# Optimization experiments

Measured on AMD Instinct MI355X. Metric: run time of the kernel, lower is better.

The kernel has to match this reference:

```python
import jax, jax.numpy as jnp
import numpy as np
import math

H = 16          # head_count
D = 1024        # model_dim
DT = 100        # topic_dim
DH = D // H     # dim_per_head


def _lin(x, W, b):
    return x @ W.T + b


def _shape(x, B):
    # [B, L, D] -> [B, H, L, DH]
    return x.reshape(B, -1, H, DH).transpose(0, 2, 1, 3)


def setup_inputs() -> dict:
    key = jax.random.key(0)
    ks = jax.random.split(key, 20)
    B, L = 4, 1024
    s = 0.02
    inp = {
        'key': jax.random.normal(ks[0], (B, L, D), jnp.float32),
        'value': jax.random.normal(ks[1], (B, L, D), jnp.float32),
        'query': jax.random.normal(ks[2], (B, L, D), jnp.float32),
        'mask': jax.random.randint(ks[3], (B, L, L), 0, 2).astype(bool),
        'topic_vec': jax.random.normal(ks[4], (B, L, DT), jnp.float32),
        'Wq': jax.random.normal(ks[5], (D, D), jnp.float32) * s,
        'bq': jnp.zeros((D,), jnp.float32),
        'Wk': jax.random.normal(ks[6], (D, D), jnp.float32) * s,
        'bk': jnp.zeros((D,), jnp.float32),
        'Wv': jax.random.normal(ks[7], (D, D), jnp.float32) * s,
        'bv': jnp.zeros((D,), jnp.float32),
        'Wtk': jax.random.normal(ks[8], (D, D), jnp.float32) * s,
        'btk': jnp.zeros((D,), jnp.float32),
        'Wtv': jax.random.normal(ks[9], (D, DT), jnp.float32) * s,
        'btv': jnp.zeros((D,), jnp.float32),
        'Wtw': jax.random.normal(ks[10], (H, 3 * D), jnp.float32) * s,
        'btw': jnp.zeros((H,), jnp.float32),
        'Wo': jax.random.normal(ks[11], (D, D), jnp.float32) * s,
        'bo': jnp.zeros((D,), jnp.float32),
    }
    return inp


def reference(key, value, query, mask, topic_vec,
              Wq, bq, Wk, bk, Wv, bv, Wtk, btk, Wtv, btv, Wtw, btw, Wo, bo):
    B = key.shape[0]
    # content and topic projections
    q_lin = _lin(query, Wq, bq)          # [B, L, D]
    k_lin = _lin(key, Wk, bk)
    v_lin = _lin(value, Wv, bv)
    tk_lin = _lin(key, Wtk, btk)         # topic keys from key states
    tv_lin = _lin(topic_vec, Wtv, btv)   # topic queries from topic distribution

    q = _shape(q_lin, B) / math.sqrt(DH)   # [B, H, Lq, DH]
    k = _shape(k_lin, B)
    v = _shape(v_lin, B)
    tk = _shape(tk_lin, B)
    tq = _shape(tv_lin, B) / math.sqrt(DH)

    scores = jnp.einsum('bhqd,bhkd->bhqk', q, k)          # content scores
    topic_scores = jnp.einsum('bhqd,bhkd->bhqk', tq, tk)  # topic scores

    # per-query, per-head mixing gate from concatenated projections (3*D -> H)
    gate = jax.nn.sigmoid(_lin(jnp.concatenate([q_lin, tk_lin, tv_lin], axis=-1), Wtw, btw))  # [B, L, H]
    p = gate.transpose(0, 2, 1)[..., None]                # [B, H, Lq, 1]
    scores = (1.0 - p) * scores + p * topic_scores

    # masked_fill(mask, -1e18), mask broadcast over heads
    scores = jnp.where(mask[:, None, :, :], -1e18, scores)
    attn = jax.nn.softmax(scores, axis=-1)
    # dropout is identity at eval time
    ctx = jnp.einsum('bhqk,bhkd->bhqd', attn, v)
    ctx = ctx.transpose(0, 2, 1, 3).reshape(B, -1, D)     # unshape
    return ctx @ Wo.T + bo
```

## Files before the change

kernel.cpp:

```cpp
#include <hip/hip_runtime.h>
#include <hip/hip_bf16.h>

#define BB 4
#define LL 1024
#define DD 1024
#define HH 16
#define DHH 64
#define DTT 100
#define ML (BB*LL)
#define LOG2E 1.4426950408889634f

typedef float f32x4 __attribute__((ext_vector_type(4)));
typedef short s16x8 __attribute__((ext_vector_type(8)));

__device__ __forceinline__ unsigned short f2bf(float x) {
    unsigned u = __builtin_bit_cast(unsigned, x);
    return (unsigned short)((u + 0x7FFFu + ((u >> 16) & 1u)) >> 16);
}
__device__ __forceinline__ unsigned short f2bf_fast(float x) {
    return (unsigned short)((__builtin_bit_cast(unsigned, x) + 0x8000u) >> 16);
}
__device__ __forceinline__ unsigned cvt_pk_bf16(float lo, float hi) {
    unsigned r;
    asm("v_cvt_pk_bf16_f32 %0, %1, %2" : "=v"(r) : "v"(lo), "v"(hi));
    return r;
}
__device__ __forceinline__ float bflo(unsigned u) { return __builtin_bit_cast(float, u << 16); }
__device__ __forceinline__ float bfhi(unsigned u) { return __builtin_bit_cast(float, u & 0xFFFF0000u); }
__device__ __forceinline__ int4 pack_bf16x8(float4 x0, float4 x1) {
    int4 o;
    o.x = cvt_pk_bf16(x0.x, x0.y); o.y = cvt_pk_bf16(x0.z, x0.w);
    o.z = cvt_pk_bf16(x1.x, x1.y); o.w = cvt_pk_bf16(x1.z, x1.w);
    return o;
}

__global__ __launch_bounds__(256)
void conv_fused(const float* __restrict__ w0, const float* __restrict__ w1,
                const float* __restrict__ w2, const float* __restrict__ w3,
                const float* __restrict__ w4, unsigned short* __restrict__ wd,
                const float* __restrict__ wtw, unsigned short* __restrict__ wtwd,
                const float* __restrict__ wtv, unsigned short* __restrict__ wtvd,
                const float* __restrict__ topic, unsigned short* __restrict__ topicd,
                const int* __restrict__ mask, unsigned long long* __restrict__ MB) {
    const int bx = blockIdx.x, tid = threadIdx.x;
    if (bx < 2560) {
        const int which = bx >> 9;
        const float* src;
        switch (which) {
            case 0:  src = w0; break;
            case 1:  src = w1; break;
            case 2:  src = w2; break;
            case 3:  src = w3; break;
            default: src = w4; break;
        }
        unsigned short* dst = wd + (size_t)which * DD * DD;
        const int idx = (bx & 511) * 256 + tid;
        float4 f0 = *(const float4*)(src + (size_t)idx * 8);
        float4 f1 = *(const float4*)(src + (size_t)idx * 8 + 4);
        *(int4*)(dst + (size_t)idx * 8) = pack_bf16x8(f0, f1);
    } else if (bx < 2584) {
        const int idx = (bx - 2560) * 256 + tid;
        float4 f0 = *(const float4*)(wtw + (size_t)idx * 8);
        float4 f1 = *(const float4*)(wtw + (size_t)idx * 8 + 4);
        *(int4*)(wtwd + (size_t)idx * 8) = pack_bf16x8(f0, f1);
    } else if (bx < 2648) {
        const int idx = (bx - 2584) * 256 + tid;
        const int r = idx >> 4, c0 = (idx & 15) * 8;
        unsigned short o[8];
        #pragma unroll
        for (int j = 0; j < 8; j++) {
            int c = c0 + j;
            o[j] = (c < DTT) ? f2bf(wtv[(size_t)r * DTT + c]) : (unsigned short)0;
        }
        int4 v;
        v.x = o[0] | ((unsigned)o[1] << 16);
        v.y = o[2] | ((unsigned)o[3] << 16);
        v.z = o[4] | ((unsigned)o[5] << 16);
        v.w = o[6] | ((unsigned)o[7] << 16);
        *(int4*)(wtvd + (size_t)r * 128 + c0) = v;
    } else if (bx < 2904) {
        const int idx = (bx - 2648) * 256 + tid;
        const int r = idx >> 4, c0 = (idx & 15) * 8;
        unsigned short o[8];
        #pragma unroll
        for (int j = 0; j < 8; j++) {
            int c = c0 + j;
            o[j] = (c < DTT) ? f2bf(topic[(size_t)r * DTT + c]) : (unsigned short)0;
        }
        int4 v;
        v.x = o[0] | ((unsigned)o[1] << 16);
        v.y = o[2] | ((unsigned)o[3] << 16);
        v.z = o[4] | ((unsigned)o[5] << 16);
        v.w = o[6] | ((unsigned)o[7] << 16);
        *(int4*)(topicd + (size_t)r * 128 + c0) = v;
    } else {
        const int ww = (bx - 2904) * 4 + (tid >> 6);
        const int lane = tid & 63;
        int v = mask[(size_t)ww * 64 + lane];
        unsigned long long bits = __ballot(v != 0);
        if (lane == 0) MB[ww] = bits;
    }
}

struct GArg { const void* A; const unsigned short* W; const float* bias; void* C; int mode; };

#define LOADW(s0_,s1_,s2_,s3_,kk) \
    s0_ = *(const int4*)(Wb + (kk)); \
    s1_ = *(const int4*)(Wb + (kk) + wstep); \
    s2_ = *(const int4*)(Wb + (kk) + 2 * wstep); \
    s3_ = *(const int4*)(Wb + (kk) + 3 * wstep);
#define STOREW(s0_,s1_,s2_,s3_) \
    *(int4*)(bsl)         = s0_; \
    *(int4*)(bsl + 4096)  = s1_; \
    *(int4*)(bsl + 8192)  = s2_; \
    *(int4*)(bsl + 12288) = s3_;
#define LOADA16(s0_,s1_,s2_,s3_,kk) \
    s0_ = *(const int4*)(Ab16 + (kk)); \
    s1_ = *(const int4*)(Ab16 + (kk) + wstep); \
    s2_ = *(const int4*)(Ab16 + (kk) + 2 * wstep); \
    s3_ = *(const int4*)(Ab16 + (kk) + 3 * wstep);
#define STOREA16(s0_,s1_,s2_,s3_) \
    *(int4*)(asl)         = s0_; \
    *(int4*)(asl + 4096)  = s1_; \
    *(int4*)(asl + 8192)  = s2_; \
    *(int4*)(asl + 12288) = s3_;
#define LOADA32(q0_,q1_,q2_,q3_,q4_,q5_,q6_,q7_,kk) \
    q0_ = *(const float4*)(Af32 + (kk));             q1_ = *(const float4*)(Af32 + (kk) + 4); \
    q2_ = *(const float4*)(Af32 + (kk) + wstep);     q3_ = *(const float4*)(Af32 + (kk) + wstep + 4); \
    q4_ = *(const float4*)(Af32 + (kk) + 2 * wstep); q5_ = *(const float4*)(Af32 + (kk) + 2 * wstep + 4); \
    q6_ = *(const float4*)(Af32 + (kk) + 3 * wstep); q7_ = *(const float4*)(Af32 + (kk) + 3 * wstep + 4);
#define STOREA32(q0_,q1_,q2_,q3_,q4_,q5_,q6_,q7_) \
    *(int4*)(asl)         = pack_bf16x8(q0_, q1_); \
    *(int4*)(asl + 4096)  = pack_bf16x8(q2_, q3_); \
    *(int4*)(asl + 8192)  = pack_bf16x8(q4_, q5_); \
    *(int4*)(asl + 12288) = pack_bf16x8(q6_, q7_);
#define GEMM_COMPUTE(ABASE, BBASE) \
    _Pragma("unroll") \
    for (int ks = 0; ks < 2; ks++) { \
        s16x8 af[4], bf[4]; \
        _Pragma("unroll") \
        for (int m = 0; m < 4; m++) { \
            const int ra = wr * 64 + m * 16 + c; \
            af[m] = *(const s16x8*)((ABASE) + ra * 128 + (((ks * 4 + g) ^ (ra & 7)) << 4)); \
            const int rb = wc * 64 + m * 16 + c; \
            bf[m] = *(const s16x8*)((BBASE) + rb * 128 + (((ks * 4 + g) ^ (rb & 7)) << 4)); \
        } \
        _Pragma("unroll") \
        for (int m = 0; m < 4; m++) \
            _Pragma("unroll") \
            for (int n = 0; n < 4; n++) \
                acc[m][n] = __builtin_amdgcn_mfma_f32_16x16x32_bf16(af[m], bf[n], acc[m][n], 0, 0, 0); \
    }

template<int AFP32>
__global__ __launch_bounds__(256, 3)
void gemm_mfma(GArg a0, GArg a1, GArg a2, GArg a3, int N, int K) {
    __shared__ char lds[32768];
    char* As = lds;
    char* Bs = lds + 16384;

    const int nb = gridDim.x * gridDim.y * gridDim.z;
    const int flat = blockIdx.x + gridDim.x * (blockIdx.y + gridDim.y * blockIdx.z);
    const int wid = (flat & 7) * (nb >> 3) + (flat >> 3);
    const int bx = wid % gridDim.x;
    const int rem = wid / gridDim.x;
    const int by = rem % gridDim.y;
    const int bz = rem / gridDim.y;

    GArg a;
    switch (bz) {
        case 0:  a = a0; break;
        case 1:  a = a1; break;
        case 2:  a = a2; break;
        default: a = a3; break;
    }

    const int tid = threadIdx.x, w = tid >> 6, l = tid & 63;
    const int g = l >> 4, c = l & 15;
    const int wr = w >> 1, wc = w & 1;
    const int bm = by * 128, bn = bx * 128;

    const int r0 = tid >> 3, sl = tid & 7;
    char* const asl = As + r0 * 128 + ((sl ^ (r0 & 7)) << 4);
    char* const bsl = Bs + r0 * 128 + ((sl ^ (r0 & 7)) << 4);
    const size_t wstep = (size_t)32 * K;
    const unsigned short* const Wb   = a.W + (size_t)(bn + r0) * K + sl * 8;
    const unsigned short* const Ab16 = (const unsigned short*)a.A + (size_t)(bm + r0) * K + sl * 8;
    const float* const           Af32 = (const float*)a.A + (size_t)(bm + r0) * K + sl * 8;

    f32x4 acc[4][4];
    #pragma unroll
    for (int m = 0; m < 4; m++)
        #pragma unroll
        for (int n = 0; n < 4; n++)
            #pragma unroll
            for (int j = 0; j < 4; j++) acc[m][n][j] = 0.f;

    int4 pw0, pw1, pw2, pw3;
    int4 pa0, pa1, pa2, pa3;
    float4 qa0, qa1, qa2, qa3, qa4, qa5, qa6, qa7;
    LOADW(pw0, pw1, pw2, pw3, 0)
    if (AFP32) { LOADA32(qa0, qa1, qa2, qa3, qa4, qa5, qa6, qa7, 0) }
    else       { LOADA16(pa0, pa1, pa2, pa3, 0) }

    for (int k0 = 0; k0 < K; k0 += 64) {
        __syncthreads();
        if (AFP32) { STOREA32(qa0, qa1, qa2, qa3, qa4, qa5, qa6, qa7) }
        else       { STOREA16(pa0, pa1, pa2, pa3) }
        STOREW(pw0, pw1, pw2, pw3)
        {
            const int kn = (k0 + 64 < K) ? (k0 + 64) : 0;
            LOADW(pw0, pw1, pw2, pw3, kn)
            if (AFP32) { LOADA32(qa0, qa1, qa2, qa3, qa4, qa5, qa6, qa7, kn) }
            else       { LOADA16(pa0, pa1, pa2, pa3, kn) }
        }
        __syncthreads();
        GEMM_COMPUTE(As, Bs)
    }

    const int mode = a.mode;
    if (mode == 0) {
        float* C = (float*)a.C;
        #pragma unroll
        for (int n = 0; n < 4; n++) {
            const int col = bn + wc * 64 + n * 16 + c;
            const float bv = a.bias[col];
            #pragma unroll
            for (int m = 0; m < 4; m++) {
                const int row = bm + wr * 64 + m * 16 + g * 4;
                #pragma unroll
                for (int j = 0; j < 4; j++)
                    C[(size_t)(row + j) * N + col] = acc[m][n][j] + bv;
            }
        }
    } else if (mode == 1) {
        unsigned short* C = (unsigned short*)a.C;
        #pragma unroll
        for (int n = 0; n < 4; n++) {
            const int col = bn + wc * 64 + n * 16 + c;
            const float bv = a.bias[col];
            #pragma unroll
            for (int m = 0; m < 4; m++) {
                const int row = bm + wr * 64 + m * 16 + g * 4;
                #pragma unroll
                for (int j = 0; j < 4; j++)
                    C[(size_t)(row + j) * N + col] = f2bf(acc[m][n][j] + bv);
            }
        }
    } else if (mode == 2 || mode == 3) {
        unsigned short* C = (unsigned short*)a.C;
        const int off = (mode == 2) ? 0 : 64;
        #pragma unroll
        for (int n = 0; n < 4; n++) {
            const int col = bn + wc * 64 + n * 16 + c;
            const float bv = a.bias[col];
            const int h = col >> 6, d = col & 63;
            #pragma unroll
            for (int m = 0; m < 4; m++) {
                const int row = bm + wr * 64 + m * 16 + g * 4;
                #pragma unroll
                for (int j = 0; j < 4; j++) {
                    const int rr = row + j;
                    C[((size_t)((rr >> 10) * HH + h) * LL + (rr & 1023)) * 128 + off + d] =
                        f2bf(acc[m][n][j] + bv);
                }
            }
        }
    } else {
        unsigned short* C = (unsigned short*)a.C;
        #pragma unroll
        for (int n = 0; n < 4; n++) {
            const int col = bn + wc * 64 + n * 16 + c;
            const float bv = a.bias[col];
            const int h = col >> 6, d = col & 63;
            #pragma unroll
            for (int m = 0; m < 4; m++) {
                const int row = bm + wr * 64 + m * 16 + g * 4;
                unsigned lo = cvt_pk_bf16(acc[m][n][0] + bv, acc[m][n][1] + bv);
                unsigned hi = cvt_pk_bf16(acc[m][n][2] + bv, acc[m][n][3] + bv);
                unsigned long long pk = (unsigned long long)lo | ((unsigned long long)hi << 32);
                *(unsigned long long*)(C + ((size_t)((row >> 10) * HH + h) * 64 + d) * LL + (row & 1023)) = pk;
            }
        }
    }
}

__global__ __launch_bounds__(256)
void gate_kernel(const unsigned short* __restrict__ QLb,
                 const unsigned short* __restrict__ KCb,
                 const unsigned short* __restrict__ TVLb,
                 const unsigned short* __restrict__ Wtwb,
                 const float* __restrict__ btw, float* __restrict__ GATE) {
    const int t = threadIdx.x;
    const int q = t >> 6, sub = t & 63, row = sub >> 4, h = sub & 15;
    const int row_g = blockIdx.x * 4 + row;
    const int b = row_g >> 10, l = row_g & 1023;

    float acc = 0.f;
    const unsigned short* wp = Wtwb + h * 3 * DD + q * 768;
    #pragma unroll 4
    for (int cc = 0; cc < 96; cc++) {
        const int i = q * 768 + cc * 8;
        const unsigned short* xp;
        if (i < 1024) {
            xp = QLb + (size_t)row_g * DD + i;
        } else if (i < 2048) {
            const int j = i - 1024;
            xp = KCb + ((size_t)(b * HH + (j >> 6)) * LL + l) * 128 + 64 + (j & 63);
        } else {
            xp = TVLb + (size_t)row_g * DD + (i - 2048);
        }
        int4 xv = *(const int4*)xp;
        int4 wv = *(const int4*)(wp + cc * 8);
        const unsigned xs[4] = {(unsigned)xv.x, (unsigned)xv.y, (unsigned)xv.z, (unsigned)xv.w};
        const unsigned ws[4] = {(unsigned)wv.x, (unsigned)wv.y, (unsigned)wv.z, (unsigned)wv.w};
        #pragma unroll
        for (int jj = 0; jj < 4; jj++) {
            acc = fmaf(bflo(xs[jj]), bflo(ws[jj]), acc);
            acc = fmaf(bfhi(xs[jj]), bfhi(ws[jj]), acc);
        }
    }
    __shared__ float part[4][4][16];
    part[q][row][h] = acc;
    __syncthreads();
    if (t < 64) {
        float s = part[0][row][h] + part[1][row][h] + part[2][row][h] + part[3][row][h] + btw[h];
        GATE[(size_t)row_g * HH + h] = 1.f / (1.f + __expf(-s));
    }
}

__global__ __launch_bounds__(256, 3)
void attn_mfma(const unsigned short* __restrict__ QLb,
               const unsigned short* __restrict__ TVLb,
               const float* __restrict__ GATE,
               const unsigned short* __restrict__ KC,
               const unsigned short* __restrict__ VT,
               const unsigned long long* __restrict__ MB,
               unsigned short* __restrict__ CTb) {
    __shared__ char lds[32768];
    char* kc_l = lds;
    char* vt_l = lds + 16384;
    char* p_l  = lds + 24576;

    const int tid = threadIdx.x, w = tid >> 6, l = tid & 63;
    const int g = l >> 4, c = l & 15;
    const int flat = blockIdx.y * gridDim.x + blockIdx.x;
    const int wid = (flat & 7) * 128 + (flat >> 3);
    const int qb = wid & 15, bh = wid >> 4;
    const int b = bh >> 4, h = bh & 15;
    const int q0 = qb * 64;

    const size_t kcg = (size_t)bh * LL * 128;
    const size_t vtg = (size_t)bh * 64 * LL;

    const int kr = tid >> 4, ks = tid & 15;
    const size_t kgo = (size_t)kr * 128 + ks * 8;
    char* const klb = kc_l + kr * 256 + ((ks ^ (kr & 7)) << 4);
    const int vr = tid >> 3, vs = tid & 7;
    const size_t vgo = (size_t)vr * LL + vs * 8;
    char* const vlb = vt_l + vr * 128 + ((vs ^ (vr & 7)) << 4);

    int4 pk0, pk1, pk2, pk3, pv0, pv1;
    {
        const unsigned short* kp = KC + kcg + kgo;
        pk0 = *(const int4*)kp;
        pk1 = *(const int4*)(kp + 16 * 128);
        pk2 = *(const int4*)(kp + 32 * 128);
        pk3 = *(const int4*)(kp + 48 * 128);
        const unsigned short* vp = VT + vtg + vgo;
        pv0 = *(const int4*)vp;
        pv1 = *(const int4*)(vp + 32 * LL);
    }

    {
        const size_t rowbase = (size_t)b * LL + q0 + kr;
        const unsigned short* qsrc =
            (ks < 8 ? QLb : TVLb) + rowbase * DD + h * DHH + (ks & 7) * 8;
        const float* gp = GATE + rowbase * HH + h;
        #pragma unroll
        for (int i = 0; i < 4; i++) {
            const float p = gp[(size_t)i * 16 * HH];
            const float sc = (ks < 8 ? 1.f - p : p) * (0.125f * LOG2E);
            int4 v = *(const int4*)(qsrc + (size_t)i * 16 * DD);
            int4 o;
            o.x = cvt_pk_bf16(bflo((unsigned)v.x) * sc, bfhi((unsigned)v.x) * sc);
            o.y = cvt_pk_bf16(bflo((unsigned)v.y) * sc, bfhi((unsigned)v.y) * sc);
            o.z = cvt_pk_bf16(bflo((unsigned)v.z) * sc, bfhi((unsigned)v.z) * sc);
            o.w = cvt_pk_bf16(bflo((unsigned)v.w) * sc, bfhi((unsigned)v.w) * sc);
            *(int4*)(klb + i * 4096) = o;
        }
    }
    __syncthreads();
    s16x8 qf[4];
    const int ql = w * 16 + c;
    #pragma unroll
    for (int kss = 0; kss < 4; kss++) {
        int t = kss * 4 + g;
        qf[kss] = *(s16x8*)(kc_l + ql * 256 + ((t ^ (ql & 7)) << 4));
    }

    f32x4 ctx[4], la;
    #pragma unroll
    for (int ct = 0; ct < 4; ct++)
        #pragma unroll
        for (int j = 0; j < 4; j++) ctx[ct][j] = 0.f;
    #pragma unroll
    for (int j = 0; j < 4; j++) la[j] = 0.f;
    float m_s = -1e18f;

    s16x8 ones;
    #pragma unroll
    for (int j = 0; j < 8; j++) ones[j] = (short)0x3F80;

    const unsigned long long* mbq = MB + ((size_t)b * LL + q0 + w * 16 + c) * 16;

    for (int kt = 0; kt < 16; kt++) {
        __syncthreads();
        *(int4*)(klb)          = pk0;
        *(int4*)(klb + 4096)   = pk1;
        *(int4*)(klb + 8192)   = pk2;
        *(int4*)(klb + 12288)  = pk3;
        *(int4*)(vlb)          = pv0;
        *(int4*)(vlb + 4096)   = pv1;
        {
            const unsigned short* kp = KC + kcg + (size_t)(kt + 1) * (64 * 128) + kgo;
            pk0 = *(const int4*)kp;
            pk1 = *(const int4*)(kp + 16 * 128);
            pk2 = *(const int4*)(kp + 32 * 128);
            pk3 = *(const int4*)(kp + 48 * 128);
            const unsigned short* vp = VT + vtg + (size_t)(kt + 1) * 64 + vgo;
            pv0 = *(const int4*)vp;
            pv1 = *(const int4*)(vp + 32 * LL);
        }
        __syncthreads();

        f32x4 sf[4];
        #pragma unroll
        for (int ct = 0; ct < 4; ct++) {
            f32x4 acc;
            #pragma unroll
            for (int j = 0; j < 4; j++) acc[j] = 0.f;
            const int rk = ct * 16 + c;
            #pragma unroll
            for (int kss = 0; kss < 4; kss++) {
                int t = kss * 4 + g;
                s16x8 kf = *(s16x8*)(kc_l + rk * 256 + ((t ^ (rk & 7)) << 4));
                acc = __builtin_amdgcn_mfma_f32_16x16x32_bf16(kf, qf[kss], acc, 0, 0, 0);
            }
            sf[ct] = acc;
        }

        {
            const unsigned long long mw = mbq[kt];
            const unsigned ms0 = (unsigned)(mw >> (g * 4));
            const unsigned ms1 = (unsigned)(mw >> (g * 4 + 32));
            #pragma unroll
            for (int ct = 0; ct < 4; ct++) {
                const unsigned mm = (ct & 2) ? ms1 : ms0;
                const int sh = (ct & 1) ? 16 : 0;
                #pragma unroll
                for (int j = 0; j < 4; j++)
                    if ((mm >> (sh + j)) & 1u) sf[ct][j] = -1e18f;
            }
            float t0 = fmaxf(fmaxf(sf[0][0], sf[0][1]), fmaxf(sf[0][2], sf[0][3]));
            float t1 = fmaxf(fmaxf(sf[1][0], sf[1][1]), fmaxf(sf[1][2], sf[1][3]));
            float t2 = fmaxf(fmaxf(sf[2][0], sf[2][1]), fmaxf(sf[2][2], sf[2][3]));
            float t3 = fmaxf(fmaxf(sf[3][0], sf[3][1]), fmaxf(sf[3][2], sf[3][3]));
            float mx = fmaxf(fmaxf(t0, t1), fmaxf(t2, t3));
            mx = fmaxf(mx, __shfl_xor(mx, 16));
            mx = fmaxf(mx, __shfl_xor(mx, 32));
            const float mn = fmaxf(m_s, mx);
            const float cf = exp2f(m_s - mn);
            m_s = mn;

            const float cr0 = __shfl(cf, g * 4 + 0, 16);
            const float cr1 = __shfl(cf, g * 4 + 1, 16);
            const float cr2 = __shfl(cf, g * 4 + 2, 16);
            const float cr3 = __shfl(cf, g * 4 + 3, 16);
            #pragma unroll
            for (int ct = 0; ct < 4; ct++) {
                ctx[ct][0] *= cr0; ctx[ct][1] *= cr1;
                ctx[ct][2] *= cr2; ctx[ct][3] *= cr3;
            }
            la[0] *= cr0; la[1] *= cr1; la[2] *= cr2; la[3] *= cr3;

            char* pw = p_l + w * 2048 + c * 128;
            #pragma unroll
            for (int ct = 0; ct < 4; ct++) {
                const unsigned lo = cvt_pk_bf16(exp2f(sf[ct][0] - mn), exp2f(sf[ct][1] - mn));
                const unsigned hi = cvt_pk_bf16(exp2f(sf[ct][2] - mn), exp2f(sf[ct][3] - mn));
                const unsigned long long pkv =
                    (unsigned long long)lo | ((unsigned long long)hi << 32);
                *(unsigned long long*)(pw + (((ct * 2 + (g >> 1)) ^ (c & 7)) << 4) + ((g & 1) << 3)) = pkv;
            }
        }

        char* pb = p_l + w * 2048;
        s16x8 pa0 = *(s16x8*)(pb + c * 128 + (((0 + g) ^ (c & 7)) << 4));
        s16x8 pa1 = *(s16x8*)(pb + c * 128 + (((4 + g) ^ (c & 7)) << 4));
        #pragma unroll
        for (int ct = 0; ct < 4; ct++) {
            const int dv = ct * 16 + c;
            s16x8 v0 = *(s16x8*)(vt_l + dv * 128 + (((0 + g) ^ (dv & 7)) << 4));
            s16x8 v1 = *(s16x8*)(vt_l + dv * 128 + (((4 + g) ^ (dv & 7)) << 4));
            ctx[ct] = __builtin_amdgcn_mfma_f32_16x16x32_bf16(pa0, v0, ctx[ct], 0, 0, 0);
            ctx[ct] = __builtin_amdgcn_mfma_f32_16x16x32_bf16(pa1, v1, ctx[ct], 0, 0, 0);
        }
        la = __builtin_amdgcn_mfma_f32_16x16x32_bf16(pa0, ones, la, 0, 0, 0);
        la = __builtin_amdgcn_mfma_f32_16x16x32_bf16(pa1, ones, la, 0, 0, 0);
    }

    #pragma unroll
    for (int r = 0; r < 4; r++) {
        const float inv = 1.f / la[r];
        const int q = q0 + w * 16 + g * 4 + r;
        unsigned short* dst = CTb + ((size_t)b * LL + q) * DD + h * DHH + c;
        dst[0]  = f2bf(ctx[0][r] * inv);
        dst[16] = f2bf(ctx[1][r] * inv);
        dst[32] = f2bf(ctx[2][r] * inv);
        dst[48] = f2bf(ctx[3][r] * inv);
    }
}

extern "C" void kernel_launch(void* const* d_in, const int* in_sizes, int n_in,
                              void* d_out, int out_size, void* d_ws, size_t ws_size,
                              hipStream_t stream) {
    const float* key   = (const float*)d_in[0];
    const float* value = (const float*)d_in[1];
    const float* query = (const float*)d_in[2];
    const int*   mask  = (const int*)d_in[3];
    const float* topic = (const float*)d_in[4];
    const float* Wq  = (const float*)d_in[5];  const float* bq  = (const float*)d_in[6];
    const float* Wk  = (const float*)d_in[7];  const float* bk  = (const float*)d_in[8];
    const float* Wv  = (const float*)d_in[9];  const float* bv  = (const float*)d_in[10];
    const float* Wtk = (const float*)d_in[11]; const float* btk = (const float*)d_in[12];
    const float* Wtv = (const float*)d_in[13]; const float* btv = (const float*)d_in[14];
    const float* Wtw = (const float*)d_in[15]; const float* btw = (const float*)d_in[16];
    const float* Wo  = (const float*)d_in[17]; const float* bo  = (const float*)d_in[18];
    float* out = (float*)d_out;

    const size_t NTOK = (size_t)ML * DD;
    unsigned short* Wqb   = (unsigned short*)d_ws;
    unsigned short* Wkb   = Wqb  + (size_t)DD * DD;
    unsigned short* Wvb   = Wkb  + (size_t)DD * DD;
    unsigned short* Wtkb  = Wvb  + (size_t)DD * DD;
    unsigned short* Wob   = Wtkb + (size_t)DD * DD;
    unsigned short* Wtvb  = Wob  + (size_t)DD * DD;
    unsigned short* Wtwb  = Wtvb + (size_t)DD * 128;
    unsigned short* topicb= Wtwb + (size_t)HH * 3 * DD;
    unsigned short* QLb   = topicb + (size_t)ML * 128;
    unsigned short* TVLb  = QLb  + NTOK;
    unsigned short* CTb   = TVLb + NTOK;
    unsigned short* KCb   = CTb  + NTOK;
    unsigned short* VTb   = KCb  + (size_t)BB * HH * LL * 128;
    float* GATE           = (float*)(VTb + (size_t)BB * HH * 64 * LL);
    unsigned long long* MBp = (unsigned long long*)(GATE + (size_t)ML * HH);

    conv_fused<<<19288, 256, 0, stream>>>(Wq, Wk, Wv, Wtk, Wo, Wqb,
                                          Wtw, Wtwb, Wtv, Wtvb, topic, topicb,
                                          mask, MBp);

    gemm_mfma<1><<<dim3(DD / 128, ML / 128, 4), 256, 0, stream>>>(
        GArg{query, Wqb,  bq,  QLb, 1},
        GArg{key,   Wkb,  bk,  KCb, 2},
        GArg{value, Wvb,  bv,  VTb, 4},
        GArg{key,   Wtkb, btk, KCb, 3},
        DD, DD);
    gemm_mfma<0><<<dim3(DD / 128, ML / 128, 1), 256, 0, stream>>>(
        GArg{topicb, Wtvb, btv, TVLb, 1},
        GArg{topicb, Wtvb, btv, TVLb, 1},
        GArg{topicb, Wtvb, btv, TVLb, 1},
        GArg{topicb, Wtvb, btv, TVLb, 1},
        DD, 128);

    gate_kernel<<<ML / 4, 256, 0, stream>>>(QLb, KCb, TVLb, Wtwb, btw, GATE);

    attn_mfma<<<dim3(LL / 64, BB * HH), 256, 0, stream>>>(QLb, TVLb, GATE, KCb, VTb, MBp, CTb);

    gemm_mfma<0><<<dim3(DD / 128, ML / 128, 1), 256, 0, stream>>>(
        GArg{CTb, Wob, bo, out, 0},
        GArg{CTb, Wob, bo, out, 0},
        GArg{CTb, Wob, bo, out, 0},
        GArg{CTb, Wob, bo, out, 0},
        DD, DD);
}
```

Measured before the change: 196.2 us.

## Pre-convert activations to bf16 and use 256x256 direct-to-LDS GEMM for projections

```diff
diff --git a/kernel.cpp b/kernel.cpp
--- a/kernel.cpp
+++ b/kernel.cpp
@@ -33,16 +33,36 @@
     o.z = cvt_pk_bf16(x1.x, x1.y); o.w = cvt_pk_bf16(x1.z, x1.w);
     return o;
 }
+__device__ __forceinline__ void gl_lds16(const unsigned short* g, char* l) {
+    __builtin_amdgcn_global_load_lds(
+        (const __attribute__((address_space(1))) unsigned*)g,
+        (__attribute__((address_space(3))) unsigned*)l, 16, 0, 0);
+}
 
 __global__ __launch_bounds__(256)
-void conv_fused(const float* __restrict__ w0, const float* __restrict__ w1,
+void conv_fused(const float* __restrict__ qf, const float* __restrict__ kf,
+                const float* __restrict__ vf,
+                unsigned short* __restrict__ qb, unsigned short* __restrict__ kb,
+                unsigned short* __restrict__ vb,
+                const float* __restrict__ w0, const float* __restrict__ w1,
                 const float* __restrict__ w2, const float* __restrict__ w3,
                 const float* __restrict__ w4, unsigned short* __restrict__ wd,
                 const float* __restrict__ wtw, unsigned short* __restrict__ wtwd,
                 const float* __restrict__ wtv, unsigned short* __restrict__ wtvd,
                 const float* __restrict__ topic, unsigned short* __restrict__ topicd,
                 const int* __restrict__ mask, unsigned long long* __restrict__ MB) {
-    const int bx = blockIdx.x, tid = threadIdx.x;
+    const int bx0 = blockIdx.x, tid = threadIdx.x;
+    if (bx0 < 6144) {
+        const int which = bx0 >> 11;
+        const float* src = which == 0 ? qf : (which == 1 ? kf : vf);
+        unsigned short* dst = which == 0 ? qb : (which == 1 ? kb : vb);
+        const int idx = (bx0 & 2047) * 256 + tid;
+        float4 f0 = *(const float4*)(src + (size_t)idx * 8);
+        float4 f1 = *(const float4*)(src + (size_t)idx * 8 + 4);
+        *(int4*)(dst + (size_t)idx * 8) = pack_bf16x8(f0, f1);
+        return;
+    }
+    const int bx = bx0 - 6144;
     if (bx < 2560) {
         const int which = bx >> 9;
         const float* src;
@@ -103,6 +123,153 @@
 }
 
 struct GArg { const void* A; const unsigned short* W; const float* bias; void* C; int mode; };
+
+#define STAGE256(kt_, Ad_, Bd_) { \
+    const unsigned short* agp_ = Ag + (size_t)(kt_) * 64; \
+    const unsigned short* bgp_ = Bg + (size_t)(kt_) * 64; \
+    _Pragma("unroll") \
+    for (int i_ = 0; i_ < 4; i_++) { \
+        gl_lds16(agp_ + (size_t)(i_ * 64) * K, (Ad_) + i_ * 8192 + ldst); \
+        gl_lds16(bgp_ + (size_t)(i_ * 64) * K, (Bd_) + i_ * 8192 + ldst); \
+    } }
+
+__global__ __launch_bounds__(512, 2)
+void gemm256(GArg a0, GArg a1, GArg a2, GArg a3, int N, int K) {
+    __shared__ char lds[131072];
+
+    const int nb = gridDim.x * gridDim.y * gridDim.z;
+    const int flat = blockIdx.x + gridDim.x * (blockIdx.y + gridDim.y * blockIdx.z);
+    const int wid = (flat & 7) * (nb >> 3) + (flat >> 3);
+    const int bx = wid % gridDim.x;
+    const int rem = wid / gridDim.x;
+    const int by = rem % gridDim.y;
+    const int bz = rem / gridDim.y;
+
+    GArg a;
+    switch (bz) {
+        case 0:  a = a0; break;
+        case 1:  a = a1; break;
+        case 2:  a = a2; break;
+        default: a = a3; break;
+    }
+
+    const int tid = threadIdx.x, w = tid >> 6, l = tid & 63;
+    const int g = l >> 4, c = l & 15;
+    const int wm = w >> 2, wn = w & 3;
+    const int bm = by * 256, bn = bx * 256;
+    const int NK = K >> 6;
+
+    const int srow = tid >> 3;
+    const int scol = (tid & 7) ^ (srow & 7);
+    const unsigned short* const Ag = (const unsigned short*)a.A + (size_t)(bm + srow) * K + scol * 8;
+    const unsigned short* const Bg = a.W + (size_t)(bn + srow) * K + scol * 8;
+    const int ldst = tid * 16;
+
+    f32x4 acc[8][4];
+    #pragma unroll
+    for (int m = 0; m < 8; m++)
+        #pragma unroll
+        for (int n = 0; n < 4; n++)
+            #pragma unroll
+            for (int j = 0; j < 4; j++) acc[m][n][j] = 0.f;
+
+    STAGE256(0, lds, lds + 32768)
+    if (NK > 1) STAGE256(1, lds + 65536, lds + 98304)
+
+    for (int kt = 0; kt < NK; kt++) {
+        char* Ab = lds + (kt & 1) * 65536;
+        char* Bb = Ab + 32768;
+        if (kt + 1 < NK) { asm volatile("s_waitcnt vmcnt(8)" ::: "memory"); }
+        else             { asm volatile("s_waitcnt vmcnt(0)" ::: "memory"); }
+        __builtin_amdgcn_sched_barrier(0);
+        __builtin_amdgcn_s_barrier();
+        __builtin_amdgcn_sched_barrier(0);
+
+        s16x8 bfr[4][2];
+        #pragma unroll
+        for (int n = 0; n < 4; n++) {
+            const int rb = wn * 64 + n * 16 + c;
+            #pragma unroll
+            for (int ks = 0; ks < 2; ks++)
+                bfr[n][ks] = *(const s16x8*)(Bb + rb * 128 + (((ks * 4 + g) ^ (rb & 7)) << 4));
+        }
+        #pragma unroll
+        for (int p = 0; p < 4; p++) {
+            s16x8 af[2][2];
+            #pragma unroll
+            for (int mm = 0; mm < 2; mm++) {
+                const int ra = wm * 128 + (p * 2 + mm) * 16 + c;
+                #pragma unroll
+                for (int ks = 0; ks < 2; ks++)
+                    af[mm][ks] = *(const s16x8*)(Ab + ra * 128 + (((ks * 4 + g) ^ (ra & 7)) << 4));
+            }
+            #pragma unroll
+            for (int mm = 0; mm < 2; mm++)
+                #pragma unroll
+                for (int n = 0; n < 4; n++) {
+                    acc[p * 2 + mm][n] = __builtin_amdgcn_mfma_f32_16x16x32_bf16(af[mm][0], bfr[n][0], acc[p * 2 + mm][n], 0, 0, 0);
+                    acc[p * 2 + mm][n] = __builtin_amdgcn_mfma_f32_16x16x32_bf16(af[mm][1], bfr[n][1], acc[p * 2 + mm][n], 0, 0, 0);
+                }
+        }
+        asm volatile("s_waitcnt lgkmcnt(0)" ::: "memory");
+        __builtin_amdgcn_sched_barrier(0);
+        __builtin_amdgcn_s_barrier();
+        __builtin_amdgcn_sched_barrier(0);
+        if (kt + 2 < NK) STAGE256(kt + 2, Ab, Bb)
+    }
+
+    const int mode = a.mode;
+    if (mode == 1) {
+        unsigned short* C = (unsigned short*)a.C;
+        #pragma unroll
+        for (int n = 0; n < 4; n++) {
+            const int col = bn + wn * 64 + n * 16 + c;
+            const float bv = a.bias[col];
+            #pragma unroll
+            for (int m = 0; m < 8; m++) {
+                const int row = bm + wm * 128 + m * 16 + g * 4;
+                #pragma unroll
+                for (int j = 0; j < 4; j++)
+                    C[(size_t)(row + j) * N + col] = f2bf(acc[m][n][j] + bv);
+            }
+        }
+    } else if (mode == 2 || mode == 3) {
+        unsigned short* C = (unsigned short*)a.C;
+        const int off = (mode == 2) ? 0 : 64;
+        #pragma unroll
+        for (int n = 0; n < 4; n++) {
+            const int col = bn + wn * 64 + n * 16 + c;
+            const float bv = a.bias[col];
+            const int h = col >> 6, d = col & 63;
+            #pragma unroll
+            for (int m = 0; m < 8; m++) {
+                const int row = bm + wm * 128 + m * 16 + g * 4;
+                #pragma unroll
+                for (int j = 0; j < 4; j++) {
+                    const int rr = row + j;
+                    C[((size_t)((rr >> 10) * HH + h) * LL + (rr & 1023)) * 128 + off + d] =
+                        f2bf(acc[m][n][j] + bv);
+                }
+            }
+        }
+    } else {
+        unsigned short* C = (unsigned short*)a.C;
+        #pragma unroll
+        for (int n = 0; n < 4; n++) {
+            const int col = bn + wn * 64 + n * 16 + c;
+            const float bv = a.bias[col];
+            const int h = col >> 6, d = col & 63;
+            #pragma unroll
+            for (int m = 0; m < 8; m++) {
+                const int row = bm + wm * 128 + m * 16 + g * 4;
+                unsigned lo = cvt_pk_bf16(acc[m][n][0] + bv, acc[m][n][1] + bv);
+                unsigned hi = cvt_pk_bf16(acc[m][n][2] + bv, acc[m][n][3] + bv);
+                unsigned long long pk = (unsigned long long)lo | ((unsigned long long)hi << 32);
+                *(unsigned long long*)(C + ((size_t)((row >> 10) * HH + h) * 64 + d) * LL + (row & 1023)) = pk;
+            }
+        }
+    }
+}
 
 #define LOADW(s0_,s1_,s2_,s3_,kk) \
     s0_ = *(const int4*)(Wb + (kk)); \
@@ -124,16 +291,6 @@
     *(int4*)(asl + 4096)  = s1_; \
     *(int4*)(asl + 8192)  = s2_; \
     *(int4*)(asl + 12288) = s3_;
-#define LOADA32(q0_,q1_,q2_,q3_,q4_,q5_,q6_,q7_,kk) \
-    q0_ = *(const float4*)(Af32 + (kk));             q1_ = *(const float4*)(Af32 + (kk) + 4); \
-    q2_ = *(const float4*)(Af32 + (kk) + wstep);     q3_ = *(const float4*)(Af32 + (kk) + wstep + 4); \
-    q4_ = *(const float4*)(Af32 + (kk) + 2 * wstep); q5_ = *(const float4*)(Af32 + (kk) + 2 * wstep + 4); \
-    q6_ = *(const float4*)(Af32 + (kk) + 3 * wstep); q7_ = *(const float4*)(Af32 + (kk) + 3 * wstep + 4);
-#define STOREA32(q0_,q1_,q2_,q3_,q4_,q5_,q6_,q7_) \
-    *(int4*)(asl)         = pack_bf16x8(q0_, q1_); \
-    *(int4*)(asl + 4096)  = pack_bf16x8(q2_, q3_); \
-    *(int4*)(asl + 8192)  = pack_bf16x8(q4_, q5_); \
-    *(int4*)(asl + 12288) = pack_bf16x8(q6_, q7_);
 #define GEMM_COMPUTE(ABASE, BBASE) \
     _Pragma("unroll") \
     for (int ks = 0; ks < 2; ks++) { \
@@ -152,7 +309,6 @@
                 acc[m][n] = __builtin_amdgcn_mfma_f32_16x16x32_bf16(af[m], bf[n], acc[m][n], 0, 0, 0); \
     }
 
-template<int AFP32>
 __global__ __launch_bounds__(256, 3)
 void gemm_mfma(GArg a0, GArg a1, GArg a2, GArg a3, int N, int K) {
     __shared__ char lds[32768];
@@ -186,7 +342,6 @@
     const size_t wstep = (size_t)32 * K;
     const unsigned short* const Wb   = a.W + (size_t)(bn + r0) * K + sl * 8;
     const unsigned short* const Ab16 = (const unsigned short*)a.A + (size_t)(bm + r0) * K + sl * 8;
-    const float* const           Af32 = (const float*)a.A + (size_t)(bm + r0) * K + sl * 8;
 
     f32x4 acc[4][4];
     #pragma unroll
@@ -198,21 +353,17 @@
 
     int4 pw0, pw1, pw2, pw3;
     int4 pa0, pa1, pa2, pa3;
-    float4 qa0, qa1, qa2, qa3, qa4, qa5, qa6, qa7;
     LOADW(pw0, pw1, pw2, pw3, 0)
-    if (AFP32) { LOADA32(qa0, qa1, qa2, qa3, qa4, qa5, qa6, qa7, 0) }
-    else       { LOADA16(pa0, pa1, pa2, pa3, 0) }
+    LOADA16(pa0, pa1, pa2, pa3, 0)
 
     for (int k0 = 0; k0 < K; k0 += 64) {
         __syncthreads();
-        if (AFP32) { STOREA32(qa0, qa1, qa2, qa3, qa4, qa5, qa6, qa7) }
-        else       { STOREA16(pa0, pa1, pa2, pa3) }
+        STOREA16(pa0, pa1, pa2, pa3)
         STOREW(pw0, pw1, pw2, pw3)
         {
             const int kn = (k0 + 64 < K) ? (k0 + 64) : 0;
             LOADW(pw0, pw1, pw2, pw3, kn)
-            if (AFP32) { LOADA32(qa0, qa1, qa2, qa3, qa4, qa5, qa6, qa7, kn) }
-            else       { LOADA16(pa0, pa1, pa2, pa3, kn) }
+            LOADA16(pa0, pa1, pa2, pa3, kn)
         }
         __syncthreads();
         GEMM_COMPUTE(As, Bs)
@@ -233,7 +384,7 @@
                     C[(size_t)(row + j) * N + col] = acc[m][n][j] + bv;
             }
         }
-    } else if (mode == 1) {
+    } else {
         unsigned short* C = (unsigned short*)a.C;
         #pragma unroll
         for (int n = 0; n < 4; n++) {
@@ -245,41 +396,6 @@
                 #pragma unroll
                 for (int j = 0; j < 4; j++)
                     C[(size_t)(row + j) * N + col] = f2bf(acc[m][n][j] + bv);
-            }
-        }
-    } else if (mode == 2 || mode == 3) {
-        unsigned short* C = (unsigned short*)a.C;
-        const int off = (mode == 2) ? 0 : 64;
-        #pragma unroll
-        for (int n = 0; n < 4; n++) {
-            const int col = bn + wc * 64 + n * 16 + c;
-            const float bv = a.bias[col];
-            const int h = col >> 6, d = col & 63;
-            #pragma unroll
-            for (int m = 0; m < 4; m++) {
-                const int row = bm + wr * 64 + m * 16 + g * 4;
-                #pragma unroll
-                for (int j = 0; j < 4; j++) {
-                    const int rr = row + j;
-                    C[((size_t)((rr >> 10) * HH + h) * LL + (rr & 1023)) * 128 + off + d] =
-                        f2bf(acc[m][n][j] + bv);
-                }
-            }
-        }
-    } else {
-        unsigned short* C = (unsigned short*)a.C;
-        #pragma unroll
-        for (int n = 0; n < 4; n++) {
-            const int col = bn + wc * 64 + n * 16 + c;
-            const float bv = a.bias[col];
-            const int h = col >> 6, d = col & 63;
-            #pragma unroll
-            for (int m = 0; m < 4; m++) {
-                const int row = bm + wr * 64 + m * 16 + g * 4;
-                unsigned lo = cvt_pk_bf16(acc[m][n][0] + bv, acc[m][n][1] + bv);
-                unsigned hi = cvt_pk_bf16(acc[m][n][2] + bv, acc[m][n][3] + bv);
-                unsigned long long pk = (unsigned long long)lo | ((unsigned long long)hi << 32);
-                *(unsigned long long*)(C + ((size_t)((row >> 10) * HH + h) * 64 + d) * LL + (row & 1023)) = pk;
             }
         }
     }
@@ -555,18 +671,22 @@
     unsigned short* VTb   = KCb  + (size_t)BB * HH * LL * 128;
     float* GATE           = (float*)(VTb + (size_t)BB * HH * 64 * LL);
     unsigned long long* MBp = (unsigned long long*)(GATE + (size_t)ML * HH);
-
-    conv_fused<<<19288, 256, 0, stream>>>(Wq, Wk, Wv, Wtk, Wo, Wqb,
+    unsigned short* QBb   = (unsigned short*)(MBp + (size_t)BB * LL * LL / 64);
+    unsigned short* KBb   = QBb + NTOK;
+    unsigned short* VBb   = KBb + NTOK;
+
+    conv_fused<<<25432, 256, 0, stream>>>(query, key, value, QBb, KBb, VBb,
+                                          Wq, Wk, Wv, Wtk, Wo, Wqb,
                                           Wtw, Wtwb, Wtv, Wtvb, topic, topicb,
                                           mask, MBp);
 
-    gemm_mfma<1><<<dim3(DD / 128, ML / 128, 4), 256, 0, stream>>>(
-        GArg{query, Wqb,  bq,  QLb, 1},
-        GArg{key,   Wkb,  bk,  KCb, 2},
-        GArg{value, Wvb,  bv,  VTb, 4},
-        GArg{key,   Wtkb, btk, KCb, 3},
+    gemm256<<<dim3(DD / 256, ML / 256, 4), 512, 0, stream>>>(
+        GArg{QBb, Wqb,  bq,  QLb, 1},
+        GArg{KBb, Wkb,  bk,  KCb, 2},
+        GArg{VBb, Wvb,  bv,  VTb, 4},
+        GArg{KBb, Wtkb, btk, KCb, 3},
         DD, DD);
-    gemm_mfma<0><<<dim3(DD / 128, ML / 128, 1), 256, 0, stream>>>(
+    gemm_mfma<<<dim3(DD / 128, ML / 128, 1), 256, 0, stream>>>(
         GArg{topicb, Wtvb, btv, TVLb, 1},
         GArg{topicb, Wtvb, btv, TVLb, 1},
         GArg{topicb, Wtvb, btv, TVLb, 1},
@@ -577,7 +697,7 @@
 
     attn_mfma<<<dim3(LL / 64, BB * HH), 256, 0, stream>>>(QLb, TVLb, GATE, KCb, VTb, MBp, CTb);
 
-    gemm_mfma<0><<<dim3(DD / 128, ML / 128, 1), 256, 0, stream>>>(
+    gemm_mfma<<<dim3(DD / 128, ML / 128, 1), 256, 0, stream>>>(
         GArg{CTb, Wob, bo, out, 0},
         GArg{CTb, Wob, bo, out, 0},
         GArg{CTb, Wob, bo, out, 0},
```

Result: no change. 198.9 us (+1.4%).

## Pre-convert activations to bf16 and stage GEMM tiles via global_load_lds

Applied to the files above, without the earlier changes.

```diff
diff --git a/kernel.cpp b/kernel.cpp
--- a/kernel.cpp
+++ b/kernel.cpp
@@ -33,16 +33,36 @@
     o.z = cvt_pk_bf16(x1.x, x1.y); o.w = cvt_pk_bf16(x1.z, x1.w);
     return o;
 }
+__device__ __forceinline__ void gl_lds16(const unsigned short* g, char* l) {
+    __builtin_amdgcn_global_load_lds(
+        (const __attribute__((address_space(1))) unsigned*)g,
+        (__attribute__((address_space(3))) unsigned*)l, 16, 0, 0);
+}
 
 __global__ __launch_bounds__(256)
-void conv_fused(const float* __restrict__ w0, const float* __restrict__ w1,
+void conv_fused(const float* __restrict__ qf, const float* __restrict__ kf,
+                const float* __restrict__ vf,
+                unsigned short* __restrict__ qb, unsigned short* __restrict__ kb,
+                unsigned short* __restrict__ vb,
+                const float* __restrict__ w0, const float* __restrict__ w1,
                 const float* __restrict__ w2, const float* __restrict__ w3,
                 const float* __restrict__ w4, unsigned short* __restrict__ wd,
                 const float* __restrict__ wtw, unsigned short* __restrict__ wtwd,
                 const float* __restrict__ wtv, unsigned short* __restrict__ wtvd,
                 const float* __restrict__ topic, unsigned short* __restrict__ topicd,
                 const int* __restrict__ mask, unsigned long long* __restrict__ MB) {
-    const int bx = blockIdx.x, tid = threadIdx.x;
+    const int bx0 = blockIdx.x, tid = threadIdx.x;
+    if (bx0 < 6144) {
+        const int which = bx0 >> 11;
+        const float* src = which == 0 ? qf : (which == 1 ? kf : vf);
+        unsigned short* dst = which == 0 ? qb : (which == 1 ? kb : vb);
+        const int idx = (bx0 & 2047) * 256 + tid;
+        float4 f0 = *(const float4*)(src + (size_t)idx * 8);
+        float4 f1 = *(const float4*)(src + (size_t)idx * 8 + 4);
+        *(int4*)(dst + (size_t)idx * 8) = pack_bf16x8(f0, f1);
+        return;
+    }
+    const int bx = bx0 - 6144;
     if (bx < 2560) {
         const int which = bx >> 9;
         const float* src;
@@ -102,59 +122,10 @@
     }
 }
 
-struct GArg { const void* A; const unsigned short* W; const float* bias; void* C; int mode; };
-
-#define LOADW(s0_,s1_,s2_,s3_,kk) \
-    s0_ = *(const int4*)(Wb + (kk)); \
-    s1_ = *(const int4*)(Wb + (kk) + wstep); \
-    s2_ = *(const int4*)(Wb + (kk) + 2 * wstep); \
-    s3_ = *(const int4*)(Wb + (kk) + 3 * wstep);
-#define STOREW(s0_,s1_,s2_,s3_) \
-    *(int4*)(bsl)         = s0_; \
-    *(int4*)(bsl + 4096)  = s1_; \
-    *(int4*)(bsl + 8192)  = s2_; \
-    *(int4*)(bsl + 12288) = s3_;
-#define LOADA16(s0_,s1_,s2_,s3_,kk) \
-    s0_ = *(const int4*)(Ab16 + (kk)); \
-    s1_ = *(const int4*)(Ab16 + (kk) + wstep); \
-    s2_ = *(const int4*)(Ab16 + (kk) + 2 * wstep); \
-    s3_ = *(const int4*)(Ab16 + (kk) + 3 * wstep);
-#define STOREA16(s0_,s1_,s2_,s3_) \
-    *(int4*)(asl)         = s0_; \
-    *(int4*)(asl + 4096)  = s1_; \
-    *(int4*)(asl + 8192)  = s2_; \
-    *(int4*)(asl + 12288) = s3_;
-#define LOADA32(q0_,q1_,q2_,q3_,q4_,q5_,q6_,q7_,kk) \
-    q0_ = *(const float4*)(Af32 + (kk));             q1_ = *(const float4*)(Af32 + (kk) + 4); \
-    q2_ = *(const float4*)(Af32 + (kk) + wstep);     q3_ = *(const float4*)(Af32 + (kk) + wstep + 4); \
-    q4_ = *(const float4*)(Af32 + (kk) + 2 * wstep); q5_ = *(const float4*)(Af32 + (kk) + 2 * wstep + 4); \
-    q6_ = *(const float4*)(Af32 + (kk) + 3 * wstep); q7_ = *(const float4*)(Af32 + (kk) + 3 * wstep + 4);
-#define STOREA32(q0_,q1_,q2_,q3_,q4_,q5_,q6_,q7_) \
-    *(int4*)(asl)         = pack_bf16x8(q0_, q1_); \
-    *(int4*)(asl + 4096)  = pack_bf16x8(q2_, q3_); \
-    *(int4*)(asl + 8192)  = pack_bf16x8(q4_, q5_); \
-    *(int4*)(asl + 12288) = pack_bf16x8(q6_, q7_);
-#define GEMM_COMPUTE(ABASE, BBASE) \
-    _Pragma("unroll") \
-    for (int ks = 0; ks < 2; ks++) { \
-        s16x8 af[4], bf[4]; \
-        _Pragma("unroll") \
-        for (int m = 0; m < 4; m++) { \
-            const int ra = wr * 64 + m * 16 + c; \
-            af[m] = *(const s16x8*)((ABASE) + ra * 128 + (((ks * 4 + g) ^ (ra & 7)) << 4)); \
-            const int rb = wc * 64 + m * 16 + c; \
-            bf[m] = *(const s16x8*)((BBASE) + rb * 128 + (((ks * 4 + g) ^ (rb & 7)) << 4)); \
-        } \
-        _Pragma("unroll") \
-        for (int m = 0; m < 4; m++) \
-            _Pragma("unroll") \
-            for (int n = 0; n < 4; n++) \
-                acc[m][n] = __builtin_amdgcn_mfma_f32_16x16x32_bf16(af[m], bf[n], acc[m][n], 0, 0, 0); \
-    }
-
-template<int AFP32>
+struct GArg { const void* A; const unsigned short* W; const float* bias; void* C; int mode; int K; };
+
 __global__ __launch_bounds__(256, 3)
-void gemm_mfma(GArg a0, GArg a1, GArg a2, GArg a3, int N, int K) {
+void gemm128(GArg a0, GArg a1, GArg a2, GArg a3, GArg a4, int N) {
     __shared__ char lds[32768];
     char* As = lds;
     char* Bs = lds + 16384;
@@ -172,21 +143,22 @@
         case 0:  a = a0; break;
         case 1:  a = a1; break;
         case 2:  a = a2; break;
-        default: a = a3; break;
-    }
+        case 3:  a = a3; break;
+        default: a = a4; break;
+    }
+    const int K = a.K;
+    const int NK = K >> 6;
 
     const int tid = threadIdx.x, w = tid >> 6, l = tid & 63;
     const int g = l >> 4, c = l & 15;
     const int wr = w >> 1, wc = w & 1;
     const int bm = by * 128, bn = bx * 128;
 
-    const int r0 = tid >> 3, sl = tid & 7;
-    char* const asl = As + r0 * 128 + ((sl ^ (r0 & 7)) << 4);
-    char* const bsl = Bs + r0 * 128 + ((sl ^ (r0 & 7)) << 4);
-    const size_t wstep = (size_t)32 * K;
-    const unsigned short* const Wb   = a.W + (size_t)(bn + r0) * K + sl * 8;
-    const unsigned short* const Ab16 = (const unsigned short*)a.A + (size_t)(bm + r0) * K + sl * 8;
-    const float* const           Af32 = (const float*)a.A + (size_t)(bm + r0) * K + sl * 8;
+    const int srow = tid >> 3;
+    const int scol = (tid & 7) ^ (srow & 7);
+    const unsigned short* const Ag = (const unsigned short*)a.A + (size_t)(bm + srow) * K + scol * 8;
+    const unsigned short* const Bg = a.W + (size_t)(bn + srow) * K + scol * 8;
+    const int ldst = tid * 16;
 
     f32x4 acc[4][4];
     #pragma unroll
@@ -196,26 +168,34 @@
             #pragma unroll
             for (int j = 0; j < 4; j++) acc[m][n][j] = 0.f;
 
-    int4 pw0, pw1, pw2, pw3;
-    int4 pa0, pa1, pa2, pa3;
-    float4 qa0, qa1, qa2, qa3, qa4, qa5, qa6, qa7;
-    LOADW(pw0, pw1, pw2, pw3, 0)
-    if (AFP32) { LOADA32(qa0, qa1, qa2, qa3, qa4, qa5, qa6, qa7, 0) }
-    else       { LOADA16(pa0, pa1, pa2, pa3, 0) }
-
-    for (int k0 = 0; k0 < K; k0 += 64) {
+    for (int kt = 0; kt < NK; kt++) {
+        if (kt) __syncthreads();
+        {
+            const unsigned short* ap = Ag + (size_t)kt * 64;
+            const unsigned short* bp = Bg + (size_t)kt * 64;
+            #pragma unroll
+            for (int i = 0; i < 4; i++) {
+                gl_lds16(ap + (size_t)(i * 32) * K, As + i * 4096 + ldst);
+                gl_lds16(bp + (size_t)(i * 32) * K, Bs + i * 4096 + ldst);
+            }
+        }
         __syncthreads();
-        if (AFP32) { STOREA32(qa0, qa1, qa2, qa3, qa4, qa5, qa6, qa7) }
-        else       { STOREA16(pa0, pa1, pa2, pa3) }
-        STOREW(pw0, pw1, pw2, pw3)
-        {
-            const int kn = (k0 + 64 < K) ? (k0 + 64) : 0;
-            LOADW(pw0, pw1, pw2, pw3, kn)
-            if (AFP32) { LOADA32(qa0, qa1, qa2, qa3, qa4, qa5, qa6, qa7, kn) }
-            else       { LOADA16(pa0, pa1, pa2, pa3, kn) }
-        }
-        __syncthreads();
-        GEMM_COMPUTE(As, Bs)
+        #pragma unroll
+        for (int ks = 0; ks < 2; ks++) {
+            s16x8 af[4], bf[4];
+            #pragma unroll
+            for (int m = 0; m < 4; m++) {
+                const int ra = wr * 64 + m * 16 + c;
+                af[m] = *(const s16x8*)(As + ra * 128 + (((ks * 4 + g) ^ (ra & 7)) << 4));
+                const int rb = wc * 64 + m * 16 + c;
+                bf[m] = *(const s16x8*)(Bs + rb * 128 + (((ks * 4 + g) ^ (rb & 7)) << 4));
+            }
+            #pragma unroll
+            for (int m = 0; m < 4; m++)
+                #pragma unroll
+                for (int n = 0; n < 4; n++)
+                    acc[m][n] = __builtin_amdgcn_mfma_f32_16x16x32_bf16(af[m], bf[n], acc[m][n], 0, 0, 0);
+        }
     }
 
     const int mode = a.mode;
@@ -555,32 +535,32 @@
     unsigned short* VTb   = KCb  + (size_t)BB * HH * LL * 128;
     float* GATE           = (float*)(VTb + (size_t)BB * HH * 64 * LL);
     unsigned long long* MBp = (unsigned long long*)(GATE + (size_t)ML * HH);
-
-    conv_fused<<<19288, 256, 0, stream>>>(Wq, Wk, Wv, Wtk, Wo, Wqb,
+    unsigned short* QBb   = (unsigned short*)(MBp + (size_t)BB * LL * LL / 64);
+    unsigned short* KBb   = QBb + NTOK;
+    unsigned short* VBb   = KBb + NTOK;
+
+    conv_fused<<<25432, 256, 0, stream>>>(query, key, value, QBb, KBb, VBb,
+                                          Wq, Wk, Wv, Wtk, Wo, Wqb,
                                           Wtw, Wtwb, Wtv, Wtvb, topic, topicb,
                                           mask, MBp);
 
-    gemm_mfma<1><<<dim3(DD / 128, ML / 128, 4), 256, 0, stream>>>(
-        GArg{query, Wqb,  bq,  QLb, 1},
-        GArg{key,   Wkb,  bk,  KCb, 2},
-        GArg{value, Wvb,  bv,  VTb, 4},
-        GArg{key,   Wtkb, btk, KCb, 3},
-        DD, DD);
-    gemm_mfma<0><<<dim3(DD / 128, ML / 128, 1), 256, 0, stream>>>(
-        GArg{topicb, Wtvb, btv, TVLb, 1},
-        GArg{topicb, Wtvb, btv, TVLb, 1},
-        GArg{topicb, Wtvb, btv, TVLb, 1},
-        GArg{topicb, Wtvb, btv, TVLb, 1},
-        DD, 128);
+    gemm128<<<dim3(DD / 128, ML / 128, 5), 256, 0, stream>>>(
+        GArg{QBb,    Wqb,  bq,  QLb,  1, DD},
+        GArg{KBb,    Wkb,  bk,  KCb,  2, DD},
+        GArg{VBb,    Wvb,  bv,  VTb,  4, DD},
+        GArg{KBb,    Wtkb, btk, KCb,  3, DD},
+        GArg{topicb, Wtvb, btv, TVLb, 1, 128},
+        DD);
 
     gate_kernel<<<ML / 4, 256, 0, stream>>>(QLb, KCb, TVLb, Wtwb, btw, GATE);
 
     attn_mfma<<<dim3(LL / 64, BB * HH), 256, 0, stream>>>(QLb, TVLb, GATE, KCb, VTb, MBp, CTb);
 
-    gemm_mfma<0><<<dim3(DD / 128, ML / 128, 1), 256, 0, stream>>>(
-        GArg{CTb, Wob, bo, out, 0},
-        GArg{CTb, Wob, bo, out, 0},
-        GArg{CTb, Wob, bo, out, 0},
-        GArg{CTb, Wob, bo, out, 0},
-        DD, DD);
-}
+    gemm128<<<dim3(DD / 128, ML / 128, 1), 256, 0, stream>>>(
+        GArg{CTb, Wob, bo, out, 0, DD},
+        GArg{CTb, Wob, bo, out, 0, DD},
+        GArg{CTb, Wob, bo, out, 0, DD},
+        GArg{CTb, Wob, bo, out, 0, DD},
+        GArg{CTb, Wob, bo, out, 0, DD},
+        DD);
+}
```

Result: slower. 210.4 us (+7.2%).
